# Optimization experiments

Hardware: AMD Instinct MI355X
Metric: run time of the kernel (lower is better)

The kernel has to match this reference:

```python
import jax, jax.numpy as jnp
import numpy as np

N_NODES = 100000
N_EDGES = 800000
D_IN = 128
D_OUT = 128


def setup_inputs() -> dict:
    key = jax.random.key(0)
    k1, k2, k3, k4 = jax.random.split(key, 4)
    x = jax.random.normal(k1, (N_NODES, D_IN), dtype=jnp.float32)
    edge_index = jax.random.randint(k2, (2, N_EDGES), 0, N_NODES, dtype=jnp.int32)
    # torch Linear convention: W is [out_dim, in_dim]
    W = jax.random.normal(k3, (D_OUT, D_IN), dtype=jnp.float32) * (1.0 / np.sqrt(D_IN))
    b = jax.random.normal(k4, (D_OUT,), dtype=jnp.float32) * 0.01
    return {"x": x, "edge_index": edge_index, "W": W, "b": b}


def reference(x, edge_index, W, b):
    num_nodes = x.shape[0]
    row, col = edge_index[0], edge_index[1]
    loop = jnp.arange(num_nodes, dtype=row.dtype)
    # symmetrize edges and add self-loops: [2E + N] edges
    row_s = jnp.concatenate([row, col, loop])
    col_s = jnp.concatenate([col, row, loop])
    # degree via scatter-add of ones over source nodes
    deg = jax.ops.segment_sum(jnp.ones_like(row_s, dtype=x.dtype), row_s,
                              num_segments=num_nodes)
    deg_inv_sqrt = jnp.where(deg > 0, jax.lax.rsqrt(jnp.maximum(deg, 1e-30)), 0.0)
    norm = deg_inv_sqrt[row_s] * deg_inv_sqrt[col_s]  # [E_sym]
    h = x @ W.T + b  # [N, D_OUT]
    # gather source features, scale, scatter-add into destination nodes
    msgs = h[row_s] * norm[:, None]  # [E_sym, D_OUT]
    out = jax.ops.segment_sum(msgs, col_s, num_segments=num_nodes)
    return jax.nn.relu(out)
```

## Files before the change

kernel.cpp:

```cpp
#include <hip/hip_runtime.h>

#define D 128
#define NHB 256
#define MAXBUC 2048
#define WP 136

typedef __attribute__((ext_vector_type(8))) short bf16x8;
typedef __attribute__((ext_vector_type(4))) float f32x4;

__device__ inline ushort f2b(float f) {
  unsigned u = __float_as_uint(f);
  return (ushort)((u + 0x7fffu + ((u >> 16) & 1u)) >> 16);
}

__global__ __launch_bounds__(256) void k_gemm3(
    const float* __restrict__ x, const float* __restrict__ W,
    const float* __restrict__ bias, ushort* __restrict__ g, int n) {
  __shared__ ushort sw[128 * WP];
  const int tid = threadIdx.x;
  const int row0 = blockIdx.x * 64;

  for (int i = tid; i < 128 * 32; i += 256) {
    int o = i >> 5, kg = i & 31;
    float4 v = ((const float4*)W)[i];
    ushort4 h;
    h.x = f2b(v.x); h.y = f2b(v.y); h.z = f2b(v.z); h.w = f2b(v.w);
    *(ushort4*)(&sw[o * WP + kg * 4]) = h;
  }
  __syncthreads();

  const int wid = tid >> 6, lane = tid & 63;
  const int wr0 = wid * 16;
  const int col = lane & 15, quad = lane >> 4;
  int arow = row0 + wr0 + col;
  if (arow >= n) arow = n - 1;
  const float4* xrow = (const float4*)(x + (size_t)arow * D);

  f32x4 acc[8] = {};
#pragma unroll
  for (int s = 0; s < 4; ++s) {
    float4 v0 = xrow[s * 8 + quad * 2];
    float4 v1 = xrow[s * 8 + quad * 2 + 1];
    bf16x8 a;
    a[0] = f2b(v0.x); a[1] = f2b(v0.y); a[2] = f2b(v0.z); a[3] = f2b(v0.w);
    a[4] = f2b(v1.x); a[5] = f2b(v1.y); a[6] = f2b(v1.z); a[7] = f2b(v1.w);
#pragma unroll
    for (int t = 0; t < 8; ++t) {
      bf16x8 bfr = *(const bf16x8*)(&sw[(t * 16 + col) * WP + s * 32 + quad * 8]);
      acc[t] = __builtin_amdgcn_mfma_f32_16x16x32_bf16(a, bfr, acc[t], 0, 0, 0);
    }
  }

  __syncthreads();
#pragma unroll
  for (int t = 0; t < 8; ++t) {
    float bcol = bias[t * 16 + col];
#pragma unroll
    for (int r = 0; r < 4; ++r) {
      int row = wr0 + quad * 4 + r;
      sw[row * WP + t * 16 + col] = f2b(acc[t][r] + bcol);
    }
  }
  __syncthreads();
  for (int i = tid; i < 64 * 16; i += 256) {
    int r = i >> 4, c = i & 15;
    int gr = row0 + r;
    if (gr < n)
      *(uint4*)(&g[(size_t)gr * D + c * 8]) = *(const uint4*)(&sw[r * WP + c * 8]);
  }
}

__global__ __launch_bounds__(256) void k_hist(const int* __restrict__ ei,
                                              int* __restrict__ hist,
                                              int* __restrict__ ctr, int E, int nbuc) {
  __shared__ int h[MAXBUC];
  if (blockIdx.x == 0 && threadIdx.x == 0) *ctr = 0;
  for (int i = threadIdx.x; i < nbuc; i += 256) h[i] = 0;
  __syncthreads();
  int per = (E + NHB - 1) / NHB;
  int e0 = blockIdx.x * per, e1 = min(E, e0 + per);
  for (int e = e0 + threadIdx.x; e < e1; e += 256) {
    int r = ei[e], c = ei[E + e];
    atomicAdd(&h[c >> 6], 1);
    atomicAdd(&h[r >> 6], 1);
  }
  __syncthreads();
  for (int i = threadIdx.x; i < nbuc; i += 256)
    hist[i * NHB + blockIdx.x] = h[i];
}

__global__ __launch_bounds__(256) void k_alloc(const int* __restrict__ hist,
                                               int* __restrict__ bstart,
                                               int* __restrict__ boff,
                                               int* __restrict__ bend,
                                               int* __restrict__ ctr, int nbuc) {
  int b = blockIdx.x * 4 + (threadIdx.x >> 6);
  if (b >= nbuc) return;
  int lane = threadIdx.x & 63;
  int4 v = ((const int4*)(hist + (size_t)b * NHB))[lane];
  int p1 = v.x, p2 = p1 + v.y, p3 = p2 + v.z, s = p3 + v.w;
  int incl = s;
#pragma unroll
  for (int o = 1; o < 64; o <<= 1) {
    int t = __shfl_up(incl, o);
    if (lane >= o) incl += t;
  }
  int tot = __shfl(incl, 63);
  int base = 0;
  if (lane == 63) base = atomicAdd(ctr, tot);
  base = __shfl(base, 63);
  if (lane == 63) { boff[b] = base; bend[b] = base + tot; }
  int excl = base + incl - s;
  int4 w;
  w.x = excl; w.y = excl + p1; w.z = excl + p2; w.w = excl + p3;
  ((int4*)(bstart + (size_t)b * NHB))[lane] = w;
}

__global__ __launch_bounds__(256) void k_scatter2(const int* __restrict__ ei,
                                                  const int* __restrict__ bstart,
                                                  int* __restrict__ entries,
                                                  int E, int nbuc) {
  __shared__ int cur[MAXBUC];
  for (int i = threadIdx.x; i < nbuc; i += 256)
    cur[i] = bstart[(size_t)i * NHB + blockIdx.x];
  __syncthreads();
  int per = (E + NHB - 1) / NHB;
  int e0 = blockIdx.x * per, e1 = min(E, e0 + per);
  for (int e = e0 + threadIdx.x; e < e1; e += 256) {
    int r = ei[e], c = ei[E + e];
    int p1 = atomicAdd(&cur[c >> 6], 1);
    entries[p1] = (r << 6) | (c & 63);
    int p2 = atomicAdd(&cur[r >> 6], 1);
    entries[p2] = (c << 6) | (r & 63);
  }
}

__global__ __launch_bounds__(256) void k_sortbuc(const int* __restrict__ entries,
                                                 const int* __restrict__ boff,
                                                 const int* __restrict__ bend,
                                                 int* __restrict__ srcs,
                                                 int2* __restrict__ nodese,
                                                 float* __restrict__ dis, int N) {
  __shared__ int bin[64];
  __shared__ int sc[64];
  const int b = blockIdx.x;
  const int s = boff[b], e = bend[b];

  if (threadIdx.x < 64) bin[threadIdx.x] = 0;
  __syncthreads();
  for (int i = s + threadIdx.x; i < e; i += 256)
    atomicAdd(&bin[entries[i] & 63], 1);
  __syncthreads();

  int v = (threadIdx.x < 64) ? bin[threadIdx.x] : 0;
  if (threadIdx.x < 64) sc[threadIdx.x] = v;
  __syncthreads();
  for (int o = 1; o < 64; o <<= 1) {
    int t = (threadIdx.x < 64 && threadIdx.x >= (unsigned)o) ? sc[threadIdx.x - o] : 0;
    __syncthreads();
    if (threadIdx.x < 64) sc[threadIdx.x] += t;
    __syncthreads();
  }
  if (threadIdx.x < 64) {
    int start = s + sc[threadIdx.x] - v;
    bin[threadIdx.x] = start;
    int gn = b * 64 + threadIdx.x;
    if (gn < N) {
      nodese[gn] = make_int2(start, v);
      dis[gn] = rsqrtf((float)(v + 1));
    }
  }
  __syncthreads();

  for (int i = s + threadIdx.x; i < e; i += 256) {
    int en = entries[i];
    int p = atomicAdd(&bin[en & 63], 1);
    srcs[p] = en >> 6;
  }
}

__global__ __launch_bounds__(256) void k_agg5(const int2* __restrict__ nodese,
                                              const int* __restrict__ srcs,
                                              const uint* __restrict__ g32,
                                              const float* __restrict__ dis,
                                              float* __restrict__ out, int N) {
  int w = blockIdx.x * 4 + (threadIdx.x >> 6);
  if (w >= N) return;
  int lane = threadIdx.x & 63;

  float dv = dis[w];
  uint us = g32[(size_t)w * 64 + lane];
  float ax = __uint_as_float(us << 16) * dv;
  float ay = __uint_as_float(us & 0xffff0000u) * dv;

  int2 se = nodese[w];
  int s = se.x, e = se.x + se.y;
  for (int base = s; base < e; base += 64) {
    int cnt = e - base; if (cnt > 64) cnt = 64;
    int idx = base + lane;
    int my = (idx < e) ? srcs[idx] : 0;
    float dl = (idx < e) ? dis[my] : 0.f;
    int k = 0;
    for (; k + 7 < cnt; k += 8) {
      int u0 = __shfl(my, k);     int u1 = __shfl(my, k + 1);
      int u2 = __shfl(my, k + 2); int u3 = __shfl(my, k + 3);
      int u4 = __shfl(my, k + 4); int u5 = __shfl(my, k + 5);
      int u6 = __shfl(my, k + 6); int u7 = __shfl(my, k + 7);
      float d0 = __shfl(dl, k);     float d1 = __shfl(dl, k + 1);
      float d2 = __shfl(dl, k + 2); float d3 = __shfl(dl, k + 3);
      float d4 = __shfl(dl, k + 4); float d5 = __shfl(dl, k + 5);
      float d6 = __shfl(dl, k + 6); float d7 = __shfl(dl, k + 7);
      uint a0 = g32[(size_t)u0 * 64 + lane];
      uint a1 = g32[(size_t)u1 * 64 + lane];
      uint a2 = g32[(size_t)u2 * 64 + lane];
      uint a3 = g32[(size_t)u3 * 64 + lane];
      uint a4 = g32[(size_t)u4 * 64 + lane];
      uint a5 = g32[(size_t)u5 * 64 + lane];
      uint a6 = g32[(size_t)u6 * 64 + lane];
      uint a7 = g32[(size_t)u7 * 64 + lane];
      ax = fmaf(d0, __uint_as_float(a0 << 16), ax);
      ay = fmaf(d0, __uint_as_float(a0 & 0xffff0000u), ay);
      ax = fmaf(d1, __uint_as_float(a1 << 16), ax);
      ay = fmaf(d1, __uint_as_float(a1 & 0xffff0000u), ay);
      ax = fmaf(d2, __uint_as_float(a2 << 16), ax);
      ay = fmaf(d2, __uint_as_float(a2 & 0xffff0000u), ay);
      ax = fmaf(d3, __uint_as_float(a3 << 16), ax);
      ay = fmaf(d3, __uint_as_float(a3 & 0xffff0000u), ay);
      ax = fmaf(d4, __uint_as_float(a4 << 16), ax);
      ay = fmaf(d4, __uint_as_float(a4 & 0xffff0000u), ay);
      ax = fmaf(d5, __uint_as_float(a5 << 16), ax);
      ay = fmaf(d5, __uint_as_float(a5 & 0xffff0000u), ay);
      ax = fmaf(d6, __uint_as_float(a6 << 16), ax);
      ay = fmaf(d6, __uint_as_float(a6 & 0xffff0000u), ay);
      ax = fmaf(d7, __uint_as_float(a7 << 16), ax);
      ay = fmaf(d7, __uint_as_float(a7 & 0xffff0000u), ay);
    }
    for (; k < cnt; ++k) {
      int u = __shfl(my, k);
      float du = __shfl(dl, k);
      uint a = g32[(size_t)u * 64 + lane];
      ax = fmaf(du, __uint_as_float(a << 16), ax);
      ay = fmaf(du, __uint_as_float(a & 0xffff0000u), ay);
    }
  }
  float2 o;
  o.x = fmaxf(ax * dv, 0.f);
  o.y = fmaxf(ay * dv, 0.f);
  ((float2*)out)[(size_t)w * 64 + lane] = o;
}

extern "C" void kernel_launch(void* const* d_in, const int* in_sizes, int n_in,
                              void* d_out, int out_size, void* d_ws, size_t ws_size,
                              hipStream_t stream) {
  const float* x  = (const float*)d_in[0];
  const int*   ei = (const int*)d_in[1];
  const float* W  = (const float*)d_in[2];
  const float* b  = (const float*)d_in[3];
  float* out = (float*)d_out;

  const int N = in_sizes[0] / D;
  const int E = in_sizes[1] / 2;
  const int NBUC = (N + 63) / 64;

  char* ws = (char*)d_ws;
  size_t off = 0;
  ushort* g    = (ushort*)(ws + off); off += (size_t)N * D * 2;
  off = (off + 255) & ~(size_t)255;
  float* dis   = (float*)(ws + off);  off += (size_t)N * 4;
  off = (off + 255) & ~(size_t)255;
  int2* nodese = (int2*)(ws + off);   off += (size_t)N * 8;
  off = (off + 255) & ~(size_t)255;
  int* boff    = (int*)(ws + off);    off += (size_t)NBUC * 4;
  int* bend    = (int*)(ws + off);    off += (size_t)NBUC * 4;
  int* ctr     = (int*)(ws + off);    off += 256;
  off = (off + 255) & ~(size_t)255;
  int* hist    = (int*)(ws + off);    off += (size_t)NBUC * NHB * 4;
  off = (off + 255) & ~(size_t)255;
  int* bstart  = (int*)(ws + off);    off += (size_t)NBUC * NHB * 4;
  off = (off + 255) & ~(size_t)255;
  int* entries = (int*)(ws + off);    off += (size_t)2 * E * 4;
  off = (off + 255) & ~(size_t)255;
  int* srcs    = (int*)(ws + off);    off += (size_t)2 * E * 4;

  k_gemm3<<<NBUC, 256, 0, stream>>>(x, W, b, g, N);
  k_hist<<<NHB, 256, 0, stream>>>(ei, hist, ctr, E, NBUC);
  k_alloc<<<(NBUC + 3) / 4, 256, 0, stream>>>(hist, bstart, boff, bend, ctr, NBUC);
  k_scatter2<<<NHB, 256, 0, stream>>>(ei, bstart, entries, E, NBUC);
  k_sortbuc<<<NBUC, 256, 0, stream>>>(entries, boff, bend, srcs, nodese, dis, N);
  k_agg5<<<(N + 3) / 4, 256, 0, stream>>>(nodese, srcs, (const uint*)g, dis, out, N);
}
```

Baseline: 235.1 us.

## Replace bucketed two-level CSR build with per-node atomic counting sort

```diff
diff --git a/kernel.cpp b/kernel.cpp
--- a/kernel.cpp
+++ b/kernel.cpp
@@ -1,9 +1,8 @@
 #include <hip/hip_runtime.h>
 
 #define D 128
-#define NHB 256
-#define MAXBUC 2048
 #define WP 136
+#define DEGB 512
 
 typedef __attribute__((ext_vector_type(8))) short bf16x8;
 typedef __attribute__((ext_vector_type(4))) float f32x4;
@@ -13,12 +12,24 @@
   return (ushort)((u + 0x7fffu + ((u >> 16) & 1u)) >> 16);
 }
 
-__global__ __launch_bounds__(256) void k_gemm3(
+__global__ __launch_bounds__(256) void k_gemm_deg(
     const float* __restrict__ x, const float* __restrict__ W,
-    const float* __restrict__ bias, ushort* __restrict__ g, int n) {
+    const float* __restrict__ bias, ushort* __restrict__ g, int n,
+    const int* __restrict__ ei, int* __restrict__ deg, int E) {
   __shared__ ushort sw[128 * WP];
+
+  if (blockIdx.x < DEGB) {
+    const int stride = DEGB * 256;
+    for (int e = blockIdx.x * 256 + threadIdx.x; e < E; e += stride) {
+      int r = ei[e], c = ei[E + e];
+      atomicAdd(&deg[r], 1);
+      atomicAdd(&deg[c], 1);
+    }
+    return;
+  }
+
   const int tid = threadIdx.x;
-  const int row0 = blockIdx.x * 64;
+  const int row0 = (blockIdx.x - DEGB) * 64;
 
   for (int i = tid; i < 128 * 32; i += 256) {
     int o = i >> 5, kg = i & 31;
@@ -70,36 +81,15 @@
   }
 }
 
-__global__ __launch_bounds__(256) void k_hist(const int* __restrict__ ei,
-                                              int* __restrict__ hist,
-                                              int* __restrict__ ctr, int E, int nbuc) {
-  __shared__ int h[MAXBUC];
-  if (blockIdx.x == 0 && threadIdx.x == 0) *ctr = 0;
-  for (int i = threadIdx.x; i < nbuc; i += 256) h[i] = 0;
-  __syncthreads();
-  int per = (E + NHB - 1) / NHB;
-  int e0 = blockIdx.x * per, e1 = min(E, e0 + per);
-  for (int e = e0 + threadIdx.x; e < e1; e += 256) {
-    int r = ei[e], c = ei[E + e];
-    atomicAdd(&h[c >> 6], 1);
-    atomicAdd(&h[r >> 6], 1);
-  }
-  __syncthreads();
-  for (int i = threadIdx.x; i < nbuc; i += 256)
-    hist[i * NHB + blockIdx.x] = h[i];
-}
-
-__global__ __launch_bounds__(256) void k_alloc(const int* __restrict__ hist,
-                                               int* __restrict__ bstart,
-                                               int* __restrict__ boff,
-                                               int* __restrict__ bend,
-                                               int* __restrict__ ctr, int nbuc) {
-  int b = blockIdx.x * 4 + (threadIdx.x >> 6);
-  if (b >= nbuc) return;
+__global__ __launch_bounds__(256) void k_alloc2(const int* __restrict__ deg,
+                                                int* __restrict__ ctr,
+                                                int2* __restrict__ nodese,
+                                                float* __restrict__ dis,
+                                                int* __restrict__ cur, int N) {
+  int n = blockIdx.x * 256 + threadIdx.x;
   int lane = threadIdx.x & 63;
-  int4 v = ((const int4*)(hist + (size_t)b * NHB))[lane];
-  int p1 = v.x, p2 = p1 + v.y, p3 = p2 + v.z, s = p3 + v.w;
-  int incl = s;
+  int d = (n < N) ? deg[n] : 0;
+  int incl = d;
 #pragma unroll
   for (int o = 1; o < 64; o <<= 1) {
     int t = __shfl_up(incl, o);
@@ -109,73 +99,24 @@
   int base = 0;
   if (lane == 63) base = atomicAdd(ctr, tot);
   base = __shfl(base, 63);
-  if (lane == 63) { boff[b] = base; bend[b] = base + tot; }
-  int excl = base + incl - s;
-  int4 w;
-  w.x = excl; w.y = excl + p1; w.z = excl + p2; w.w = excl + p3;
-  ((int4*)(bstart + (size_t)b * NHB))[lane] = w;
-}
-
-__global__ __launch_bounds__(256) void k_scatter2(const int* __restrict__ ei,
-                                                  const int* __restrict__ bstart,
-                                                  int* __restrict__ entries,
-                                                  int E, int nbuc) {
-  __shared__ int cur[MAXBUC];
-  for (int i = threadIdx.x; i < nbuc; i += 256)
-    cur[i] = bstart[(size_t)i * NHB + blockIdx.x];
-  __syncthreads();
-  int per = (E + NHB - 1) / NHB;
-  int e0 = blockIdx.x * per, e1 = min(E, e0 + per);
-  for (int e = e0 + threadIdx.x; e < e1; e += 256) {
+  int start = base + incl - d;
+  if (n < N) {
+    nodese[n] = make_int2(start, d);
+    dis[n] = rsqrtf((float)(d + 1));
+    cur[n] = start;
+  }
+}
+
+__global__ __launch_bounds__(256) void k_scatter3(const int* __restrict__ ei,
+                                                  int* __restrict__ cur,
+                                                  int* __restrict__ srcs, int E) {
+  const int stride = gridDim.x * 256;
+  for (int e = blockIdx.x * 256 + threadIdx.x; e < E; e += stride) {
     int r = ei[e], c = ei[E + e];
-    int p1 = atomicAdd(&cur[c >> 6], 1);
-    entries[p1] = (r << 6) | (c & 63);
-    int p2 = atomicAdd(&cur[r >> 6], 1);
-    entries[p2] = (c << 6) | (r & 63);
-  }
-}
-
-__global__ __launch_bounds__(256) void k_sortbuc(const int* __restrict__ entries,
-                                                 const int* __restrict__ boff,
-                                                 const int* __restrict__ bend,
-                                                 int* __restrict__ srcs,
-                                                 int2* __restrict__ nodese,
-                                                 float* __restrict__ dis, int N) {
-  __shared__ int bin[64];
-  __shared__ int sc[64];
-  const int b = blockIdx.x;
-  const int s = boff[b], e = bend[b];
-
-  if (threadIdx.x < 64) bin[threadIdx.x] = 0;
-  __syncthreads();
-  for (int i = s + threadIdx.x; i < e; i += 256)
-    atomicAdd(&bin[entries[i] & 63], 1);
-  __syncthreads();
-
-  int v = (threadIdx.x < 64) ? bin[threadIdx.x] : 0;
-  if (threadIdx.x < 64) sc[threadIdx.x] = v;
-  __syncthreads();
-  for (int o = 1; o < 64; o <<= 1) {
-    int t = (threadIdx.x < 64 && threadIdx.x >= (unsigned)o) ? sc[threadIdx.x - o] : 0;
-    __syncthreads();
-    if (threadIdx.x < 64) sc[threadIdx.x] += t;
-    __syncthreads();
-  }
-  if (threadIdx.x < 64) {
-    int start = s + sc[threadIdx.x] - v;
-    bin[threadIdx.x] = start;
-    int gn = b * 64 + threadIdx.x;
-    if (gn < N) {
-      nodese[gn] = make_int2(start, v);
-      dis[gn] = rsqrtf((float)(v + 1));
-    }
-  }
-  __syncthreads();
-
-  for (int i = s + threadIdx.x; i < e; i += 256) {
-    int en = entries[i];
-    int p = atomicAdd(&bin[en & 63], 1);
-    srcs[p] = en >> 6;
+    int p = atomicAdd(&cur[c], 1);
+    srcs[p] = r;
+    p = atomicAdd(&cur[r], 1);
+    srcs[p] = c;
   }
 }
 
@@ -270,22 +211,16 @@
   off = (off + 255) & ~(size_t)255;
   int2* nodese = (int2*)(ws + off);   off += (size_t)N * 8;
   off = (off + 255) & ~(size_t)255;
-  int* boff    = (int*)(ws + off);    off += (size_t)NBUC * 4;
-  int* bend    = (int*)(ws + off);    off += (size_t)NBUC * 4;
+  int* deg     = (int*)(ws + off);    off += (size_t)N * 4;
   int* ctr     = (int*)(ws + off);    off += 256;
   off = (off + 255) & ~(size_t)255;
-  int* hist    = (int*)(ws + off);    off += (size_t)NBUC * NHB * 4;
-  off = (off + 255) & ~(size_t)255;
-  int* bstart  = (int*)(ws + off);    off += (size_t)NBUC * NHB * 4;
-  off = (off + 255) & ~(size_t)255;
-  int* entries = (int*)(ws + off);    off += (size_t)2 * E * 4;
+  int* cur     = (int*)(ws + off);    off += (size_t)N * 4;
   off = (off + 255) & ~(size_t)255;
   int* srcs    = (int*)(ws + off);    off += (size_t)2 * E * 4;
 
-  k_gemm3<<<NBUC, 256, 0, stream>>>(x, W, b, g, N);
-  k_hist<<<NHB, 256, 0, stream>>>(ei, hist, ctr, E, NBUC);
-  k_alloc<<<(NBUC + 3) / 4, 256, 0, stream>>>(hist, bstart, boff, bend, ctr, NBUC);
-  k_scatter2<<<NHB, 256, 0, stream>>>(ei, bstart, entries, E, NBUC);
-  k_sortbuc<<<NBUC, 256, 0, stream>>>(entries, boff, bend, srcs, nodese, dis, N);
+  hipMemsetAsync(deg, 0, (size_t)N * 4 + 256, stream);
+  k_gemm_deg<<<DEGB + NBUC, 256, 0, stream>>>(x, W, b, g, N, ei, deg, E);
+  k_alloc2<<<(N + 255) / 256, 256, 0, stream>>>(deg, ctr, nodese, dis, cur, N);
+  k_scatter3<<<2048, 256, 0, stream>>>(ei, cur, srcs, E);
   k_agg5<<<(N + 3) / 4, 256, 0, stream>>>(nodese, srcs, (const uint*)g, dis, out, N);
 }
```

Result: slower. 381.3 us (+62.2%).

## Fuse bucket sort with aggregation and compute degrees via global atomics

Applied to the files above, without the earlier changes.

```diff
diff --git a/kernel.cpp b/kernel.cpp
--- a/kernel.cpp
+++ b/kernel.cpp
@@ -4,6 +4,7 @@
 #define NHB 256
 #define MAXBUC 2048
 #define WP 136
+#define CAP 2048
 
 typedef __attribute__((ext_vector_type(8))) short bf16x8;
 typedef __attribute__((ext_vector_type(4))) float f32x4;
@@ -70,9 +71,11 @@
   }
 }
 
-__global__ __launch_bounds__(256) void k_hist(const int* __restrict__ ei,
-                                              int* __restrict__ hist,
-                                              int* __restrict__ ctr, int E, int nbuc) {
+__global__ __launch_bounds__(256) void k_hist2(const int* __restrict__ ei,
+                                               int* __restrict__ hist,
+                                               int* __restrict__ ctr,
+                                               int* __restrict__ deg,
+                                               int E, int nbuc) {
   __shared__ int h[MAXBUC];
   if (blockIdx.x == 0 && threadIdx.x == 0) *ctr = 0;
   for (int i = threadIdx.x; i < nbuc; i += 256) h[i] = 0;
@@ -83,17 +86,25 @@
     int r = ei[e], c = ei[E + e];
     atomicAdd(&h[c >> 6], 1);
     atomicAdd(&h[r >> 6], 1);
+    atomicAdd(&deg[r], 1);
+    atomicAdd(&deg[c], 1);
   }
   __syncthreads();
   for (int i = threadIdx.x; i < nbuc; i += 256)
     hist[i * NHB + blockIdx.x] = h[i];
 }
 
-__global__ __launch_bounds__(256) void k_alloc(const int* __restrict__ hist,
-                                               int* __restrict__ bstart,
-                                               int* __restrict__ boff,
-                                               int* __restrict__ bend,
-                                               int* __restrict__ ctr, int nbuc) {
+__global__ __launch_bounds__(256) void k_alloc2(const int* __restrict__ hist,
+                                                int* __restrict__ bstart,
+                                                int* __restrict__ boff,
+                                                int* __restrict__ bend,
+                                                int* __restrict__ ctr,
+                                                const int* __restrict__ deg,
+                                                float* __restrict__ dis,
+                                                int nbuc, int N) {
+  int n2 = blockIdx.x * 256 + threadIdx.x;
+  if (n2 < N) dis[n2] = rsqrtf((float)(deg[n2] + 1));
+
   int b = blockIdx.x * 4 + (threadIdx.x >> 6);
   if (b >= nbuc) return;
   int lane = threadIdx.x & 63;
@@ -135,20 +146,23 @@
   }
 }
 
-__global__ __launch_bounds__(256) void k_sortbuc(const int* __restrict__ entries,
+__global__ __launch_bounds__(256) void k_aggsort(const int* __restrict__ entries,
                                                  const int* __restrict__ boff,
                                                  const int* __restrict__ bend,
-                                                 int* __restrict__ srcs,
-                                                 int2* __restrict__ nodese,
-                                                 float* __restrict__ dis, int N) {
-  __shared__ int bin[64];
-  __shared__ int sc[64];
+                                                 const uint* __restrict__ g32,
+                                                 const float* __restrict__ dis,
+                                                 int* __restrict__ gsrcs,
+                                                 float* __restrict__ out, int N) {
+  __shared__ int slds[CAP];
+  __shared__ int bin[64], sc[64], nst[64], ncn[64];
   const int b = blockIdx.x;
-  const int s = boff[b], e = bend[b];
+  const int s0 = boff[b], e0 = bend[b];
+  const int tot = e0 - s0;
+  const bool inl = (tot <= CAP);
 
   if (threadIdx.x < 64) bin[threadIdx.x] = 0;
   __syncthreads();
-  for (int i = s + threadIdx.x; i < e; i += 256)
+  for (int i = s0 + threadIdx.x; i < e0; i += 256)
     atomicAdd(&bin[entries[i] & 63], 1);
   __syncthreads();
 
@@ -162,91 +176,87 @@
     __syncthreads();
   }
   if (threadIdx.x < 64) {
-    int start = s + sc[threadIdx.x] - v;
+    int start = sc[threadIdx.x] - v;
+    nst[threadIdx.x] = start;
+    ncn[threadIdx.x] = v;
     bin[threadIdx.x] = start;
-    int gn = b * 64 + threadIdx.x;
-    if (gn < N) {
-      nodese[gn] = make_int2(start, v);
-      dis[gn] = rsqrtf((float)(v + 1));
-    }
-  }
-  __syncthreads();
-
-  for (int i = s + threadIdx.x; i < e; i += 256) {
+  }
+  __syncthreads();
+
+  for (int i = s0 + threadIdx.x; i < e0; i += 256) {
     int en = entries[i];
     int p = atomicAdd(&bin[en & 63], 1);
-    srcs[p] = en >> 6;
-  }
-}
-
-__global__ __launch_bounds__(256) void k_agg5(const int2* __restrict__ nodese,
-                                              const int* __restrict__ srcs,
-                                              const uint* __restrict__ g32,
-                                              const float* __restrict__ dis,
-                                              float* __restrict__ out, int N) {
-  int w = blockIdx.x * 4 + (threadIdx.x >> 6);
-  if (w >= N) return;
-  int lane = threadIdx.x & 63;
-
-  float dv = dis[w];
-  uint us = g32[(size_t)w * 64 + lane];
-  float ax = __uint_as_float(us << 16) * dv;
-  float ay = __uint_as_float(us & 0xffff0000u) * dv;
-
-  int2 se = nodese[w];
-  int s = se.x, e = se.x + se.y;
-  for (int base = s; base < e; base += 64) {
-    int cnt = e - base; if (cnt > 64) cnt = 64;
-    int idx = base + lane;
-    int my = (idx < e) ? srcs[idx] : 0;
-    float dl = (idx < e) ? dis[my] : 0.f;
-    int k = 0;
-    for (; k + 7 < cnt; k += 8) {
-      int u0 = __shfl(my, k);     int u1 = __shfl(my, k + 1);
-      int u2 = __shfl(my, k + 2); int u3 = __shfl(my, k + 3);
-      int u4 = __shfl(my, k + 4); int u5 = __shfl(my, k + 5);
-      int u6 = __shfl(my, k + 6); int u7 = __shfl(my, k + 7);
-      float d0 = __shfl(dl, k);     float d1 = __shfl(dl, k + 1);
-      float d2 = __shfl(dl, k + 2); float d3 = __shfl(dl, k + 3);
-      float d4 = __shfl(dl, k + 4); float d5 = __shfl(dl, k + 5);
-      float d6 = __shfl(dl, k + 6); float d7 = __shfl(dl, k + 7);
-      uint a0 = g32[(size_t)u0 * 64 + lane];
-      uint a1 = g32[(size_t)u1 * 64 + lane];
-      uint a2 = g32[(size_t)u2 * 64 + lane];
-      uint a3 = g32[(size_t)u3 * 64 + lane];
-      uint a4 = g32[(size_t)u4 * 64 + lane];
-      uint a5 = g32[(size_t)u5 * 64 + lane];
-      uint a6 = g32[(size_t)u6 * 64 + lane];
-      uint a7 = g32[(size_t)u7 * 64 + lane];
-      ax = fmaf(d0, __uint_as_float(a0 << 16), ax);
-      ay = fmaf(d0, __uint_as_float(a0 & 0xffff0000u), ay);
-      ax = fmaf(d1, __uint_as_float(a1 << 16), ax);
-      ay = fmaf(d1, __uint_as_float(a1 & 0xffff0000u), ay);
-      ax = fmaf(d2, __uint_as_float(a2 << 16), ax);
-      ay = fmaf(d2, __uint_as_float(a2 & 0xffff0000u), ay);
-      ax = fmaf(d3, __uint_as_float(a3 << 16), ax);
-      ay = fmaf(d3, __uint_as_float(a3 & 0xffff0000u), ay);
-      ax = fmaf(d4, __uint_as_float(a4 << 16), ax);
-      ay = fmaf(d4, __uint_as_float(a4 & 0xffff0000u), ay);
-      ax = fmaf(d5, __uint_as_float(a5 << 16), ax);
-      ay = fmaf(d5, __uint_as_float(a5 & 0xffff0000u), ay);
-      ax = fmaf(d6, __uint_as_float(a6 << 16), ax);
-      ay = fmaf(d6, __uint_as_float(a6 & 0xffff0000u), ay);
-      ax = fmaf(d7, __uint_as_float(a7 << 16), ax);
-      ay = fmaf(d7, __uint_as_float(a7 & 0xffff0000u), ay);
+    if (inl) slds[p] = en >> 6;
+    else     gsrcs[s0 + p] = en >> 6;
+  }
+  __syncthreads();
+
+  const int* sp = inl ? (const int*)slds : (gsrcs + s0);
+
+  const int wid = threadIdx.x >> 6, lane = threadIdx.x & 63;
+  for (int j = 0; j < 16; ++j) {
+    int ln = wid * 16 + j;
+    int gn = b * 64 + ln;
+    if (gn >= N) break;
+    int st = nst[ln], cn = ncn[ln];
+    float dv = dis[gn];
+    uint us = g32[(size_t)gn * 64 + lane];
+    float ax = __uint_as_float(us << 16) * dv;
+    float ay = __uint_as_float(us & 0xffff0000u) * dv;
+
+    for (int base = 0; base < cn; base += 64) {
+      int cnt = cn - base; if (cnt > 64) cnt = 64;
+      int idx = base + lane;
+      int my = (idx < cn) ? sp[st + idx] : 0;
+      float dl = (idx < cn) ? dis[my] : 0.f;
+      int k = 0;
+      for (; k + 7 < cnt; k += 8) {
+        int u0 = __shfl(my, k);     int u1 = __shfl(my, k + 1);
+        int u2 = __shfl(my, k + 2); int u3 = __shfl(my, k + 3);
+        int u4 = __shfl(my, k + 4); int u5 = __shfl(my, k + 5);
+        int u6 = __shfl(my, k + 6); int u7 = __shfl(my, k + 7);
+        float d0 = __shfl(dl, k);     float d1 = __shfl(dl, k + 1);
+        float d2 = __shfl(dl, k + 2); float d3 = __shfl(dl, k + 3);
+        float d4 = __shfl(dl, k + 4); float d5 = __shfl(dl, k + 5);
+        float d6 = __shfl(dl, k + 6); float d7 = __shfl(dl, k + 7);
+        uint a0 = g32[(size_t)u0 * 64 + lane];
+        uint a1 = g32[(size_t)u1 * 64 + lane];
+        uint a2 = g32[(size_t)u2 * 64 + lane];
+        uint a3 = g32[(size_t)u3 * 64 + lane];
+        uint a4 = g32[(size_t)u4 * 64 + lane];
+        uint a5 = g32[(size_t)u5 * 64 + lane];
+        uint a6 = g32[(size_t)u6 * 64 + lane];
+        uint a7 = g32[(size_t)u7 * 64 + lane];
+        ax = fmaf(d0, __uint_as_float(a0 << 16), ax);
+        ay = fmaf(d0, __uint_as_float(a0 & 0xffff0000u), ay);
+        ax = fmaf(d1, __uint_as_float(a1 << 16), ax);
+        ay = fmaf(d1, __uint_as_float(a1 & 0xffff0000u), ay);
+        ax = fmaf(d2, __uint_as_float(a2 << 16), ax);
+        ay = fmaf(d2, __uint_as_float(a2 & 0xffff0000u), ay);
+        ax = fmaf(d3, __uint_as_float(a3 << 16), ax);
+        ay = fmaf(d3, __uint_as_float(a3 & 0xffff0000u), ay);
+        ax = fmaf(d4, __uint_as_float(a4 << 16), ax);
+        ay = fmaf(d4, __uint_as_float(a4 & 0xffff0000u), ay);
+        ax = fmaf(d5, __uint_as_float(a5 << 16), ax);
+        ay = fmaf(d5, __uint_as_float(a5 & 0xffff0000u), ay);
+        ax = fmaf(d6, __uint_as_float(a6 << 16), ax);
+        ay = fmaf(d6, __uint_as_float(a6 & 0xffff0000u), ay);
+        ax = fmaf(d7, __uint_as_float(a7 << 16), ax);
+        ay = fmaf(d7, __uint_as_float(a7 & 0xffff0000u), ay);
+      }
+      for (; k < cnt; ++k) {
+        int u = __shfl(my, k);
+        float du = __shfl(dl, k);
+        uint a = g32[(size_t)u * 64 + lane];
+        ax = fmaf(du, __uint_as_float(a << 16), ax);
+        ay = fmaf(du, __uint_as_float(a & 0xffff0000u), ay);
+      }
     }
-    for (; k < cnt; ++k) {
-      int u = __shfl(my, k);
-      float du = __shfl(dl, k);
-      uint a = g32[(size_t)u * 64 + lane];
-      ax = fmaf(du, __uint_as_float(a << 16), ax);
-      ay = fmaf(du, __uint_as_float(a & 0xffff0000u), ay);
-    }
-  }
-  float2 o;
-  o.x = fmaxf(ax * dv, 0.f);
-  o.y = fmaxf(ay * dv, 0.f);
-  ((float2*)out)[(size_t)w * 64 + lane] = o;
+    float2 o;
+    o.x = fmaxf(ax * dv, 0.f);
+    o.y = fmaxf(ay * dv, 0.f);
+    ((float2*)out)[(size_t)gn * 64 + lane] = o;
+  }
 }
 
 extern "C" void kernel_launch(void* const* d_in, const int* in_sizes, int n_in,
@@ -268,11 +278,11 @@
   off = (off + 255) & ~(size_t)255;
   float* dis   = (float*)(ws + off);  off += (size_t)N * 4;
   off = (off + 255) & ~(size_t)255;
-  int2* nodese = (int2*)(ws + off);   off += (size_t)N * 8;
+  int* deg     = (int*)(ws + off);    off += (size_t)N * 4;
+  int* ctr     = (int*)(ws + off);    off += 256;
   off = (off + 255) & ~(size_t)255;
   int* boff    = (int*)(ws + off);    off += (size_t)NBUC * 4;
   int* bend    = (int*)(ws + off);    off += (size_t)NBUC * 4;
-  int* ctr     = (int*)(ws + off);    off += 256;
   off = (off + 255) & ~(size_t)255;
   int* hist    = (int*)(ws + off);    off += (size_t)NBUC * NHB * 4;
   off = (off + 255) & ~(size_t)255;
@@ -280,12 +290,12 @@
   off = (off + 255) & ~(size_t)255;
   int* entries = (int*)(ws + off);    off += (size_t)2 * E * 4;
   off = (off + 255) & ~(size_t)255;
-  int* srcs    = (int*)(ws + off);    off += (size_t)2 * E * 4;
-
+  int* gsrcs   = (int*)(ws + off);    off += (size_t)2 * E * 4;
+
+  hipMemsetAsync(deg, 0, (size_t)N * 4 + 256, stream);
   k_gemm3<<<NBUC, 256, 0, stream>>>(x, W, b, g, N);
-  k_hist<<<NHB, 256, 0, stream>>>(ei, hist, ctr, E, NBUC);
-  k_alloc<<<(NBUC + 3) / 4, 256, 0, stream>>>(hist, bstart, boff, bend, ctr, NBUC);
+  k_hist2<<<NHB, 256, 0, stream>>>(ei, hist, ctr, deg, E, NBUC);
+  k_alloc2<<<(NBUC + 3) / 4, 256, 0, stream>>>(hist, bstart, boff, bend, ctr, deg, dis, NBUC, N);
   k_scatter2<<<NHB, 256, 0, stream>>>(ei, bstart, entries, E, NBUC);
-  k_sortbuc<<<NBUC, 256, 0, stream>>>(entries, boff, bend, srcs, nodese, dis, N);
-  k_agg5<<<(N + 3) / 4, 256, 0, stream>>>(nodese, srcs, (const uint*)g, dis, out, N);
-}
+  k_aggsort<<<NBUC, 256, 0, stream>>>(entries, boff, bend, (const uint*)g, dis, gsrcs, out, N);
+}
```

Measured after the change: 290.9 us. +23.7%, slower.
